# Kernel tuning notes

Measured on AMD Instinct MI355X. Metric: run time of the kernel, lower is better.

The kernel has to match this reference:

```python
import jax, jax.numpy as jnp
import numpy as np

B, T, F, H, FC1, NC = 16384, 56, 56, 20, 128, 2


def setup_inputs() -> dict:
    key = jax.random.key(0)
    ks = jax.random.split(key, 12)
    s_in = 1.0 / np.sqrt(H)  # PyTorch GRU init scale
    d = {
        'x': jax.random.normal(ks[0], (B, T, F), jnp.float32),
        'W_ih0': jax.random.uniform(ks[1], (3 * H, F), jnp.float32, -s_in, s_in),
        'W_hh0': jax.random.uniform(ks[2], (3 * H, H), jnp.float32, -s_in, s_in),
        'b_ih0': jax.random.uniform(ks[3], (3 * H,), jnp.float32, -s_in, s_in),
        'b_hh0': jax.random.uniform(ks[4], (3 * H,), jnp.float32, -s_in, s_in),
        'W_ih1': jax.random.uniform(ks[5], (3 * H, H), jnp.float32, -s_in, s_in),
        'W_hh1': jax.random.uniform(ks[6], (3 * H, H), jnp.float32, -s_in, s_in),
        'b_ih1': jax.random.uniform(ks[7], (3 * H,), jnp.float32, -s_in, s_in),
        'b_hh1': jax.random.uniform(ks[8], (3 * H,), jnp.float32, -s_in, s_in),
        'W_fc1': jax.random.uniform(ks[9], (FC1, T * H), jnp.float32, -1 / np.sqrt(T * H), 1 / np.sqrt(T * H)),
        'b_fc1': jnp.zeros((FC1,), jnp.float32),
        'W_fc2': jax.random.uniform(ks[10], (NC, FC1), jnp.float32, -1 / np.sqrt(FC1), 1 / np.sqrt(FC1)),
        'b_fc2': jnp.zeros((NC,), jnp.float32),
    }
    return d


def gru_layer(x, W_ih, W_hh, b_ih, b_hh):
    # x: [B, T, Fin] -> output [B, T, H]; PyTorch gate order: r, z, n
    xproj = jnp.einsum('bti,gi->btg', x, W_ih) + b_ih  # [B, T, 3H]

    def step(h, xp):
        gh = h @ W_hh.T + b_hh
        i_r, i_z, i_n = jnp.split(xp, 3, axis=-1)
        h_r, h_z, h_n = jnp.split(gh, 3, axis=-1)
        r = jax.nn.sigmoid(i_r + h_r)
        z = jax.nn.sigmoid(i_z + h_z)
        n = jnp.tanh(i_n + r * h_n)
        h_new = (1.0 - z) * n + z * h
        return h_new, h_new

    h0 = jnp.zeros((x.shape[0], W_hh.shape[1]), x.dtype)
    _, ys = jax.lax.scan(step, h0, jnp.swapaxes(xproj, 0, 1))  # [T, B, H]
    return jnp.swapaxes(ys, 0, 1)


def reference(x, W_ih0, W_hh0, b_ih0, b_hh0, W_ih1, W_hh1, b_ih1, b_hh1,
              W_fc1, b_fc1, W_fc2, b_fc2):
    h1 = gru_layer(x, W_ih0, W_hh0, b_ih0, b_hh0)   # [B, T, H]
    h2 = gru_layer(h1, W_ih1, W_hh1, b_ih1, b_hh1)  # [B, T, H]
    flat = h2.reshape(h2.shape[0], -1)              # [B, T*H]
    y = flat @ W_fc1.T + b_fc1
    y = y @ W_fc2.T + b_fc2
    return y
```

## Files before the change

kernel.cpp:

```cpp
#include <hip/hip_runtime.h>


#define Bsz  16384
#define Tt   56
#define Ff   56
#define Hh   20
#define Gg   60
#define FC1n 128
#define THn  1120

#define WS_WEFF 0
#define WS_BEFF 2240

typedef __attribute__((address_space(1))) const unsigned char gas_uchar;
typedef __attribute__((address_space(3))) unsigned char las_uchar;
typedef __attribute__((ext_vector_type(2))) float f32x2;

__device__ __forceinline__ float rdlane(float v, int l) {
  return __uint_as_float(__builtin_amdgcn_readlane(__float_as_uint(v), l));
}
__device__ __forceinline__ float bperm(int addr, float v) {
  return __uint_as_float(__builtin_amdgcn_ds_bpermute(addr, __float_as_uint(v)));
}
__device__ __forceinline__ float fast_rcp(float x) { return __builtin_amdgcn_rcpf(x); }
__device__ __forceinline__ float sigmoid_fast(float x) { return fast_rcp(1.0f + __expf(-x)); }
__device__ __forceinline__ float tanh_fast(float x) { return 1.0f - 2.0f * fast_rcp(1.0f + __expf(2.0f * x)); }

__device__ __forceinline__ f32x2 mk2(float a, float b) { f32x2 r; r.x = a; r.y = b; return r; }

__device__ __forceinline__ f32x2 pkfma_s(f32x2 hs, f32x2 wv, f32x2 c) {
  f32x2 d;
  asm("v_pk_fma_f32 %0, %1, %2, %3" : "=v"(d) : "s"(hs), "v"(wv), "v"(c));
  return d;
}
__device__ __forceinline__ f32x2 pkfma_v(f32x2 a, f32x2 b, f32x2 c) {
  f32x2 d;
  asm("v_pk_fma_f32 %0, %1, %2, %3" : "=v"(d) : "v"(a), "v"(b), "v"(c));
  return d;
}
__device__ __forceinline__ f32x2 pkadd(f32x2 a, f32x2 b) {
  f32x2 d;
  asm("v_pk_add_f32 %0, %1, %2" : "=v"(d) : "v"(a), "v"(b));
  return d;
}

__device__ __forceinline__ void gru_cell(float xg, float hg, int addrR, int addrZ, float& hm) {
  float sg = sigmoid_fast(xg + hg);
  float rr = bperm(addrR, sg);
  float nn = tanh_fast(fmaf(rr, hg, xg));
  float zz = bperm(addrZ, sg);
  hm = fmaf(zz, hm - nn, nn);
}

__global__ void prep_all(const float* __restrict__ Wfc1, const float* __restrict__ bfc1,
                         const float* __restrict__ Wfc2, const float* __restrict__ bfc2,
                         float* __restrict__ ws) {
  int i = blockIdx.x * blockDim.x + threadIdx.x;
  if (i < THn) {
    float s0a = 0.f, s1a = 0.f, s0b = 0.f, s1b = 0.f;
    float s0c = 0.f, s1c = 0.f, s0d = 0.f, s1d = 0.f;
#pragma unroll 4
    for (int j = 0; j < FC1n; j += 4) {
      float wa = Wfc1[(j + 0) * THn + i];
      float wb = Wfc1[(j + 1) * THn + i];
      float wc = Wfc1[(j + 2) * THn + i];
      float wd = Wfc1[(j + 3) * THn + i];
      s0a = fmaf(wa, Wfc2[j + 0], s0a); s1a = fmaf(wa, Wfc2[FC1n + j + 0], s1a);
      s0b = fmaf(wb, Wfc2[j + 1], s0b); s1b = fmaf(wb, Wfc2[FC1n + j + 1], s1b);
      s0c = fmaf(wc, Wfc2[j + 2], s0c); s1c = fmaf(wc, Wfc2[FC1n + j + 2], s1c);
      s0d = fmaf(wd, Wfc2[j + 3], s0d); s1d = fmaf(wd, Wfc2[FC1n + j + 3], s1d);
    }
    ws[WS_WEFF + i * 2 + 0] = (s0a + s0b) + (s0c + s0d);
    ws[WS_WEFF + i * 2 + 1] = (s1a + s1b) + (s1c + s1d);
  } else if (i < THn + 2) {
    int c = i - THn;
    float s = bfc2[c];
    for (int j = 0; j < FC1n; ++j) s = fmaf(bfc1[j], Wfc2[c * FC1n + j], s);
    ws[WS_BEFF + c] = s;
  }
}

__global__ __launch_bounds__(256, 3) void gru_fused(
    const float* __restrict__ x,
    const float* __restrict__ Wih0, const float* __restrict__ bih0,
    const float* __restrict__ Whh0, const float* __restrict__ bhh0,
    const float* __restrict__ Wih1, const float* __restrict__ bih1,
    const float* __restrict__ Whh1, const float* __restrict__ bhh1,
    const float* __restrict__ ws, float* __restrict__ y) {
  __shared__ float weff[2 * THn + 2];
  __shared__ __align__(16) float xstage[4][2][2 * Ff];
  __shared__ __align__(16) float hstage[4][2][64];
  for (int idx = threadIdx.x; idx < 2 * THn + 2; idx += 256) weff[idx] = ws[idx];
  __syncthreads();

  const int lane = threadIdx.x & 63;
  const int wv = threadIdx.x >> 6;
  const int b0 = (blockIdx.x * 4 + wv) * 2;
  const int g = (lane < Gg) ? lane : 0;

  f32x2 wih0p[28], whh0p[10], wih1p[10], whh1p[10];
#pragma unroll
  for (int i = 0; i < 28; ++i) wih0p[i] = *(const f32x2*)&Wih0[g * Ff + 2 * i];
#pragma unroll
  for (int i = 0; i < 10; ++i) whh0p[i] = *(const f32x2*)&Whh0[g * Hh + 2 * i];
#pragma unroll
  for (int i = 0; i < 10; ++i) wih1p[i] = *(const f32x2*)&Wih1[g * Hh + 2 * i];
#pragma unroll
  for (int i = 0; i < 10; ++i) whh1p[i] = *(const f32x2*)&Whh1[g * Hh + 2 * i];

  const f32x2 cbi0 = mk2(bih0[g], 0.f);
  const f32x2 cb0  = mk2(bhh0[g], 0.f);
  const f32x2 cb1i = mk2(bih1[g], 0.f);
  const f32x2 cb1h = mk2(bhh1[g], 0.f);
  const f32x2 zz2  = mk2(0.f, 0.f);

  float hmA[2] = {0.f, 0.f};
  float hmB[2] = {0.f, 0.f};
  f32x2 hA2[2][10];
#pragma unroll
  for (int e = 0; e < 2; ++e)
#pragma unroll
    for (int i = 0; i < 10; ++i) hA2[e][i] = zz2;

  hstage[wv][0][lane] = 0.f;
  hstage[wv][1][lane] = 0.f;

  float ya[2] = {0.f, 0.f};
  float yb[2] = {0.f, 0.f};

  const int addrR = ((lane >= 40) ? (lane - 40) : lane) * 4;
  const int addrZ = ((lane >= 40) ? (lane - 20) : lane) * 4;
  const int jm = (lane >= 40 && lane < Gg) ? lane - 40 : 0;

  const int le = (lane >= 14) ? 1 : 0;
  const int lc = lane - le * 14;
  const float* xsrc = x + (size_t)(b0 + le) * (Tt * Ff) + lc * 4;

  if (lane < 28) {
    __builtin_amdgcn_global_load_lds((gas_uchar*)xsrc,
                                     (las_uchar*)&xstage[wv][0][0], 16, 0, 0);
  }

#pragma unroll 1
  for (int t = 0; t < Tt; ++t) {
    const float* nxt = xsrc + ((t < Tt - 1) ? Ff : 0);
    if (lane < 28) {
      __builtin_amdgcn_global_load_lds((gas_uchar*)nxt,
                                       (las_uchar*)&xstage[wv][(t + 1) & 1][0], 16, 0, 0);
    }
    asm volatile("s_waitcnt vmcnt(1)" ::: "memory");
#pragma unroll
    for (int e = 0; e < 2; ++e) {
      const float4* xb = (const float4*)&xstage[wv][t & 1][e * Ff];
      float4 q = xb[0];
      f32x2 a = pkfma_v(mk2(q.x, q.y), wih0p[0], cbi0);
      f32x2 b = pkfma_v(mk2(q.z, q.w), wih0p[1], zz2);
#pragma unroll
      for (int i = 1; i < 14; ++i) {
        q = xb[i];
        a = pkfma_v(mk2(q.x, q.y), wih0p[2 * i], a);
        b = pkfma_v(mk2(q.z, q.w), wih0p[2 * i + 1], b);
      }
      f32x2 sx = pkadd(a, b);
      f32x2 c = pkfma_s(hA2[e][0], whh0p[0], cb0);
      f32x2 d = pkfma_s(hA2[e][1], whh0p[1], zz2);
#pragma unroll
      for (int i = 2; i < 10; i += 2) {
        c = pkfma_s(hA2[e][i], whh0p[i], c);
        d = pkfma_s(hA2[e][i + 1], whh0p[i + 1], d);
      }
      f32x2 sh = pkadd(c, d);
      float xg = sx.x + sx.y;
      float hg = sh.x + sh.y;
      gru_cell(xg, hg, addrR, addrZ, hmA[e]);
#pragma unroll
      for (int i = 0; i < 10; ++i)
        hA2[e][i] = mk2(rdlane(hmA[e], 40 + 2 * i), rdlane(hmA[e], 41 + 2 * i));
    }
#pragma unroll
    for (int e = 0; e < 2; ++e) {
      f32x2 ai = pkfma_s(hA2[e][0], wih1p[0], cb1i);
      f32x2 bi = pkfma_s(hA2[e][1], wih1p[1], zz2);
#pragma unroll
      for (int i = 2; i < 10; i += 2) {
        ai = pkfma_s(hA2[e][i], wih1p[i], ai);
        bi = pkfma_s(hA2[e][i + 1], wih1p[i + 1], bi);
      }
      const float4* hb = (const float4*)&hstage[wv][e][40];
      float4 q0 = hb[0], q1 = hb[1], q2 = hb[2], q3 = hb[3], q4 = hb[4];
      f32x2 ah = pkfma_v(mk2(q0.x, q0.y), whh1p[0], cb1h);
      f32x2 bh = pkfma_v(mk2(q0.z, q0.w), whh1p[1], zz2);
      ah = pkfma_v(mk2(q1.x, q1.y), whh1p[2], ah);
      bh = pkfma_v(mk2(q1.z, q1.w), whh1p[3], bh);
      ah = pkfma_v(mk2(q2.x, q2.y), whh1p[4], ah);
      bh = pkfma_v(mk2(q2.z, q2.w), whh1p[5], bh);
      ah = pkfma_v(mk2(q3.x, q3.y), whh1p[6], ah);
      bh = pkfma_v(mk2(q3.z, q3.w), whh1p[7], bh);
      ah = pkfma_v(mk2(q4.x, q4.y), whh1p[8], ah);
      bh = pkfma_v(mk2(q4.z, q4.w), whh1p[9], bh);
      f32x2 si = pkadd(ai, bi);
      float ig = si.x + si.y;
      f32x2 sh = pkadd(ah, bh);
      float hg = sh.x + sh.y;
      gru_cell(ig, hg, addrR, addrZ, hmB[e]);
      hstage[wv][e][lane] = hmB[e];
    }
    {
      float2 wv2 = *(const float2*)&weff[(t * Hh + jm) * 2];
#pragma unroll
      for (int e = 0; e < 2; ++e) {
        ya[e] = fmaf(hmB[e], wv2.x, ya[e]);
        yb[e] = fmaf(hmB[e], wv2.y, yb[e]);
      }
    }
    xsrc += Ff;
  }

  const bool active = (lane >= 40 && lane < Gg);
#pragma unroll
  for (int e = 0; e < 2; ++e) {
    if (!active) { ya[e] = 0.f; yb[e] = 0.f; }
  }
#pragma unroll
  for (int off2 = 32; off2 >= 1; off2 >>= 1) {
#pragma unroll
    for (int e = 0; e < 2; ++e) {
      ya[e] += __shfl_xor(ya[e], off2, 64);
      yb[e] += __shfl_xor(yb[e], off2, 64);
    }
  }
  if (lane == 0) {
    float be0 = weff[WS_BEFF], be1 = weff[WS_BEFF + 1];
    float4 o0 = make_float4(ya[0] + be0, yb[0] + be1, ya[1] + be0, yb[1] + be1);
    *(float4*)(y + (size_t)b0 * 2) = o0;
  }
}

extern "C" void kernel_launch(void* const* d_in, const int* in_sizes, int n_in,
                              void* d_out, int out_size, void* d_ws, size_t ws_size,
                              hipStream_t stream) {
  const float* x    = (const float*)d_in[0];
  const float* Wih0 = (const float*)d_in[1];
  const float* Whh0 = (const float*)d_in[2];
  const float* bih0 = (const float*)d_in[3];
  const float* bhh0 = (const float*)d_in[4];
  const float* Wih1 = (const float*)d_in[5];
  const float* Whh1 = (const float*)d_in[6];
  const float* bih1 = (const float*)d_in[7];
  const float* bhh1 = (const float*)d_in[8];
  const float* Wfc1 = (const float*)d_in[9];
  const float* bfc1 = (const float*)d_in[10];
  const float* Wfc2 = (const float*)d_in[11];
  const float* bfc2 = (const float*)d_in[12];
  float* ws = (float*)d_ws;
  float* y  = (float*)d_out;

  prep_all<<<5, 256, 0, stream>>>(Wfc1, bfc1, Wfc2, bfc2, ws);
  gru_fused<<<Bsz / 8, 256, 0, stream>>>(x, Wih0, bih0, Whh0, bhh0,
                                         Wih1, bih1, Whh1, bhh1, ws, y);
}
```

Measured before the change: 517.3 us.

## Deepen x prefetch to distance two and hoist hidden matvec before wait

Extends the LDS staging buffer for x from two to four slots and prefetches two timesteps ahead, waiting with vmcnt(2) instead of vmcnt(1). The layer-0 recurrent matvec is computed before the wait so it can overlap with the outstanding load. Inline-asm packed FMA/add helpers are replaced with compiler builtins, which lets the compiler schedule them. This costs more LDS per block, which could affect occupancy at 3 blocks per CU.

```diff
diff --git a/kernel.cpp b/kernel.cpp
--- a/kernel.cpp
+++ b/kernel.cpp
@@ -15,6 +15,7 @@
 typedef __attribute__((address_space(1))) const unsigned char gas_uchar;
 typedef __attribute__((address_space(3))) unsigned char las_uchar;
 typedef __attribute__((ext_vector_type(2))) float f32x2;
+typedef __attribute__((ext_vector_type(4))) float f32x4;
 
 __device__ __forceinline__ float rdlane(float v, int l) {
   return __uint_as_float(__builtin_amdgcn_readlane(__float_as_uint(v), l));
@@ -28,19 +29,15 @@
 
 __device__ __forceinline__ f32x2 mk2(float a, float b) { f32x2 r; r.x = a; r.y = b; return r; }
 
+__device__ __forceinline__ f32x2 vfma2(f32x2 a, f32x2 b, f32x2 c) {
+  return __builtin_elementwise_fma(a, b, c);
+}
+#define LO2(q) __builtin_shufflevector((q), (q), 0, 1)
+#define HI2(q) __builtin_shufflevector((q), (q), 2, 3)
+
 __device__ __forceinline__ f32x2 pkfma_s(f32x2 hs, f32x2 wv, f32x2 c) {
   f32x2 d;
   asm("v_pk_fma_f32 %0, %1, %2, %3" : "=v"(d) : "s"(hs), "v"(wv), "v"(c));
-  return d;
-}
-__device__ __forceinline__ f32x2 pkfma_v(f32x2 a, f32x2 b, f32x2 c) {
-  f32x2 d;
-  asm("v_pk_fma_f32 %0, %1, %2, %3" : "=v"(d) : "v"(a), "v"(b), "v"(c));
-  return d;
-}
-__device__ __forceinline__ f32x2 pkadd(f32x2 a, f32x2 b) {
-  f32x2 d;
-  asm("v_pk_add_f32 %0, %1, %2" : "=v"(d) : "v"(a), "v"(b));
   return d;
 }
 
@@ -88,7 +85,7 @@
     const float* __restrict__ Whh1, const float* __restrict__ bhh1,
     const float* __restrict__ ws, float* __restrict__ y) {
   __shared__ float weff[2 * THn + 2];
-  __shared__ __align__(16) float xstage[4][2][2 * Ff];
+  __shared__ __align__(16) float xstage[4][4][2 * Ff];
   __shared__ __align__(16) float hstage[4][2][64];
   for (int idx = threadIdx.x; idx < 2 * THn + 2; idx += 256) weff[idx] = ws[idx];
   __syncthreads();
@@ -139,29 +136,21 @@
   if (lane < 28) {
     __builtin_amdgcn_global_load_lds((gas_uchar*)xsrc,
                                      (las_uchar*)&xstage[wv][0][0], 16, 0, 0);
+    __builtin_amdgcn_global_load_lds((gas_uchar*)(xsrc + Ff),
+                                     (las_uchar*)&xstage[wv][1][0], 16, 0, 0);
   }
 
 #pragma unroll 1
   for (int t = 0; t < Tt; ++t) {
-    const float* nxt = xsrc + ((t < Tt - 1) ? Ff : 0);
+    const float* nxt = xsrc + ((t + 2 < Tt) ? 2 * Ff : (size_t)(Tt - 1 - t) * Ff);
     if (lane < 28) {
       __builtin_amdgcn_global_load_lds((gas_uchar*)nxt,
-                                       (las_uchar*)&xstage[wv][(t + 1) & 1][0], 16, 0, 0);
-    }
-    asm volatile("s_waitcnt vmcnt(1)" ::: "memory");
-#pragma unroll
-    for (int e = 0; e < 2; ++e) {
-      const float4* xb = (const float4*)&xstage[wv][t & 1][e * Ff];
-      float4 q = xb[0];
-      f32x2 a = pkfma_v(mk2(q.x, q.y), wih0p[0], cbi0);
-      f32x2 b = pkfma_v(mk2(q.z, q.w), wih0p[1], zz2);
-#pragma unroll
-      for (int i = 1; i < 14; ++i) {
-        q = xb[i];
-        a = pkfma_v(mk2(q.x, q.y), wih0p[2 * i], a);
-        b = pkfma_v(mk2(q.z, q.w), wih0p[2 * i + 1], b);
-      }
-      f32x2 sx = pkadd(a, b);
+                                       (las_uchar*)&xstage[wv][(t + 2) & 3][0], 16, 0, 0);
+    }
+
+    float hg0[2];
+#pragma unroll
+    for (int e = 0; e < 2; ++e) {
       f32x2 c = pkfma_s(hA2[e][0], whh0p[0], cb0);
       f32x2 d = pkfma_s(hA2[e][1], whh0p[1], zz2);
 #pragma unroll
@@ -169,14 +158,32 @@
         c = pkfma_s(hA2[e][i], whh0p[i], c);
         d = pkfma_s(hA2[e][i + 1], whh0p[i + 1], d);
       }
-      f32x2 sh = pkadd(c, d);
+      f32x2 sh = c + d;
+      hg0[e] = sh.x + sh.y;
+    }
+
+    asm volatile("s_waitcnt vmcnt(2)" ::: "memory");
+
+#pragma unroll
+    for (int e = 0; e < 2; ++e) {
+      const f32x4* xb = (const f32x4*)&xstage[wv][t & 3][e * Ff];
+      f32x4 q = xb[0];
+      f32x2 a = vfma2(LO2(q), wih0p[0], cbi0);
+      f32x2 b = vfma2(HI2(q), wih0p[1], zz2);
+#pragma unroll
+      for (int i = 1; i < 14; ++i) {
+        q = xb[i];
+        a = vfma2(LO2(q), wih0p[2 * i], a);
+        b = vfma2(HI2(q), wih0p[2 * i + 1], b);
+      }
+      f32x2 sx = a + b;
       float xg = sx.x + sx.y;
-      float hg = sh.x + sh.y;
-      gru_cell(xg, hg, addrR, addrZ, hmA[e]);
+      gru_cell(xg, hg0[e], addrR, addrZ, hmA[e]);
 #pragma unroll
       for (int i = 0; i < 10; ++i)
         hA2[e][i] = mk2(rdlane(hmA[e], 40 + 2 * i), rdlane(hmA[e], 41 + 2 * i));
     }
+
 #pragma unroll
     for (int e = 0; e < 2; ++e) {
       f32x2 ai = pkfma_s(hA2[e][0], wih1p[0], cb1i);
@@ -186,25 +193,26 @@
         ai = pkfma_s(hA2[e][i], wih1p[i], ai);
         bi = pkfma_s(hA2[e][i + 1], wih1p[i + 1], bi);
       }
-      const float4* hb = (const float4*)&hstage[wv][e][40];
-      float4 q0 = hb[0], q1 = hb[1], q2 = hb[2], q3 = hb[3], q4 = hb[4];
-      f32x2 ah = pkfma_v(mk2(q0.x, q0.y), whh1p[0], cb1h);
-      f32x2 bh = pkfma_v(mk2(q0.z, q0.w), whh1p[1], zz2);
-      ah = pkfma_v(mk2(q1.x, q1.y), whh1p[2], ah);
-      bh = pkfma_v(mk2(q1.z, q1.w), whh1p[3], bh);
-      ah = pkfma_v(mk2(q2.x, q2.y), whh1p[4], ah);
-      bh = pkfma_v(mk2(q2.z, q2.w), whh1p[5], bh);
-      ah = pkfma_v(mk2(q3.x, q3.y), whh1p[6], ah);
-      bh = pkfma_v(mk2(q3.z, q3.w), whh1p[7], bh);
-      ah = pkfma_v(mk2(q4.x, q4.y), whh1p[8], ah);
-      bh = pkfma_v(mk2(q4.z, q4.w), whh1p[9], bh);
-      f32x2 si = pkadd(ai, bi);
+      const f32x4* hb = (const f32x4*)&hstage[wv][e][40];
+      f32x4 q0 = hb[0], q1 = hb[1], q2 = hb[2], q3 = hb[3], q4 = hb[4];
+      f32x2 ah = vfma2(LO2(q0), whh1p[0], cb1h);
+      f32x2 bh = vfma2(HI2(q0), whh1p[1], zz2);
+      ah = vfma2(LO2(q1), whh1p[2], ah);
+      bh = vfma2(HI2(q1), whh1p[3], bh);
+      ah = vfma2(LO2(q2), whh1p[4], ah);
+      bh = vfma2(HI2(q2), whh1p[5], bh);
+      ah = vfma2(LO2(q3), whh1p[6], ah);
+      bh = vfma2(HI2(q3), whh1p[7], bh);
+      ah = vfma2(LO2(q4), whh1p[8], ah);
+      bh = vfma2(HI2(q4), whh1p[9], bh);
+      f32x2 si = ai + bi;
       float ig = si.x + si.y;
-      f32x2 sh = pkadd(ah, bh);
+      f32x2 sh = ah + bh;
       float hg = sh.x + sh.y;
       gru_cell(ig, hg, addrR, addrZ, hmB[e]);
       hstage[wv][e][lane] = hmB[e];
     }
+
     {
       float2 wv2 = *(const float2*)&weff[(t * Hh + jm) * 2];
 #pragma unroll
```

After: 529.6 us. 1.02x slower.
